# Kernel optimization log

Measured on AMD Instinct MI355X. Metric: run time of the kernel, lower is better.

The kernel has to match this reference:

```python
import jax, jax.numpy as jnp
import numpy as np

B, S, H = 2, 2048, 1024
NH, DH = 16, 64
E, K, F = 8, 2, 4096
EPS = 1e-5


def _ln(x, g, b):
    mu = jnp.mean(x, axis=-1, keepdims=True)
    var = jnp.mean(jnp.square(x - mu), axis=-1, keepdims=True)
    return (x - mu) * jax.lax.rsqrt(var + EPS) * g + b


def setup_inputs() -> dict:
    key = jax.random.key(0)
    ks = jax.random.split(key, 12)
    s = 0.02
    return {
        "x": jax.random.normal(ks[0], (B, S, H), jnp.float32),
        "ln1_g": jnp.ones((H,), jnp.float32),
        "ln1_b": jnp.zeros((H,), jnp.float32),
        "qkv_w": jax.random.normal(ks[1], (3 * H, H), jnp.float32) * s,
        "qkv_b": jnp.zeros((3 * H,), jnp.float32),
        "out_w": jax.random.normal(ks[2], (H, H), jnp.float32) * s,
        "out_b": jnp.zeros((H,), jnp.float32),
        "ln2_g": jnp.ones((H,), jnp.float32),
        "ln2_b": jnp.zeros((H,), jnp.float32),
        "Wg": jax.random.normal(ks[3], (H, E), jnp.float32) * s,
        "W1": jax.random.normal(ks[4], (E, H, F), jnp.float32) * s,
        "b1": jnp.zeros((E, F), jnp.float32),
        "W2": jax.random.normal(ks[5], (E, F, H), jnp.float32) * s,
        "b2": jnp.zeros((E, H), jnp.float32),
    }


def reference(x, ln1_g, ln1_b, qkv_w, qkv_b, out_w, out_b, ln2_g, ln2_b, Wg, W1, b1, W2, b2):
    # ---- LN1 + self-attention + residual (torch MultiheadAttention, no mask) ----
    res = x
    h = _ln(x, ln1_g, ln1_b)
    qkv = h @ qkv_w.T + qkv_b                      # [B,S,3H]
    q, k, v = jnp.split(qkv, 3, axis=-1)
    q = q.reshape(B, S, NH, DH)
    k = k.reshape(B, S, NH, DH)
    v = v.reshape(B, S, NH, DH)
    scores = jnp.einsum("bqhd,bkhd->bhqk", q, k) / jnp.sqrt(jnp.float32(DH))
    attn = jax.nn.softmax(scores, axis=-1)
    o = jnp.einsum("bhqk,bkhd->bqhd", attn, v).reshape(B, S, H)
    x = o @ out_w.T + out_b + res

    # ---- LN2 + MoE FFN + residual ----
    res = x
    h = _ln(x, ln2_g, ln2_b)
    xt = h.reshape(B * S, H)                       # [T,H]
    logits = xt @ Wg                               # [T,E]
    topv, topi = jax.lax.top_k(logits, K)          # [T,K]
    w = jax.nn.softmax(topv, axis=-1)              # renormalized top-k gates
    T = B * S
    gates = jnp.zeros((T, E), xt.dtype).at[jnp.arange(T)[:, None], topi].add(w)
    # dense dispatch: per-expert first GEMM, gate-weighted combine on second
    h1 = jax.nn.gelu(jnp.einsum("th,ehf->tef", xt, W1) + b1)   # [T,E,F]
    y = jnp.einsum("tef,te,efh->th", h1, gates, W2) + gates @ b2
    return y.reshape(B, S, H) + res
```

## Files before the change

kernel.cpp:

```cpp
#include <hip/hip_runtime.h>
#include <hip/hip_bf16.h>

typedef unsigned short u16;
typedef __bf16 bf16x8 __attribute__((ext_vector_type(8)));
typedef float f32x4 __attribute__((ext_vector_type(4)));
typedef __attribute__((address_space(3))) unsigned lds_u32;
typedef __attribute__((address_space(1))) const unsigned gbl_u32;

#define DI __device__ __forceinline__

DI u16 f2b(float f) {
  unsigned u = __builtin_bit_cast(unsigned, f);
  unsigned r = (u + 0x7FFFu + ((u >> 16) & 1u)) >> 16;
  return (u16)r;
}
DI float b2f(u16 h) {
  unsigned u = ((unsigned)h) << 16;
  return __builtin_bit_cast(float, u);
}
DI float wave_sum(float v) {
#pragma unroll
  for (int o = 32; o > 0; o >>= 1) v += __shfl_down(v, o);
  return v;
}
DI float gelu_tanh(float v) {
  float u = 0.7978845608028654f * (v + 0.044715f * v * v * v);
  float eu = __expf(-2.0f * fabsf(u));
  float th = (1.0f - eu) / (1.0f + eu);
  th = (u < 0.0f) ? -th : th;
  return 0.5f * v * (1.0f + th);
}

DI void gld_lds16(const u16* g, u16* l) {
  __builtin_amdgcn_global_load_lds((gbl_u32*)g, (lds_u32*)l, 16, 0, 0);
}

template <int MT, int NT>
DI void gemm_core(const u16* __restrict__ A, long lda, const u16* __restrict__ B,
                  long ldb, int K, u16* As, u16* Bs, f32x4 acc[MT][NT]) {
  const int t = threadIdx.x, lane = t & 63, wave = t >> 6;
  const int wm = (wave >> 1) * (MT * 16), wn = (wave & 1) * (NT * 16);
  const int sr = lane >> 2;
  const int sc = (((lane & 3) ^ ((lane >> 3) & 3)) << 3);
  const int fr = lane & 15;
  const int fk = ((((lane >> 4) ^ ((fr >> 1) & 3))) << 3);
  for (int kb = 0; kb < K; kb += 32) {
#pragma unroll
    for (int ii = 0; ii < MT / 2; ++ii) {
      const int i = ii * 4 + wave;
      gld_lds16(A + (size_t)(i * 16 + sr) * lda + kb + sc, As + i * 512);
    }
#pragma unroll
    for (int ii = 0; ii < NT / 2; ++ii) {
      const int i = ii * 4 + wave;
      gld_lds16(B + (size_t)(i * 16 + sr) * ldb + kb + sc, Bs + i * 512);
    }
    __syncthreads();
    bf16x8 af[MT], bfr[NT];
#pragma unroll
    for (int m = 0; m < MT; ++m)
      af[m] = *(const bf16x8*)(As + (wm + m * 16 + fr) * 32 + fk);
#pragma unroll
    for (int n = 0; n < NT; ++n)
      bfr[n] = *(const bf16x8*)(Bs + (wn + n * 16 + fr) * 32 + fk);
#pragma unroll
    for (int m = 0; m < MT; ++m)
#pragma unroll
      for (int n = 0; n < NT; ++n)
        acc[m][n] =
            __builtin_amdgcn_mfma_f32_16x16x32_bf16(af[m], bfr[n], acc[m][n], 0, 0, 0);
    __syncthreads();
  }
}

constexpr int EP_BF16 = 0;
constexpr int EP_F32RES = 1;

template <int EP, int MT, int NT>
__global__ __launch_bounds__(256) void gemm_k(
    const u16* __restrict__ A, long lda, const u16* __restrict__ B, long ldb,
    const float* __restrict__ bias, float alpha, float* __restrict__ Cf,
    u16* __restrict__ Cb, long ldc, const float* __restrict__ resid, int K) {
  constexpr int BM = MT * 32, BN = NT * 32;
  __shared__ __align__(16) u16 As[BM * 32];
  __shared__ __align__(16) u16 Bs[BN * 32];
  const long m_base = (long)blockIdx.y * BM, n_base = (long)blockIdx.x * BN;
  const u16* Ap = A + m_base * lda;
  const u16* Bp = B + n_base * ldb;
  f32x4 acc[MT][NT];
  const f32x4 z4 = {0.f, 0.f, 0.f, 0.f};
#pragma unroll
  for (int m = 0; m < MT; ++m)
#pragma unroll
    for (int n = 0; n < NT; ++n) acc[m][n] = z4;
  gemm_core<MT, NT>(Ap, lda, Bp, ldb, K, As, Bs, acc);
  const int lane = threadIdx.x & 63, wave = threadIdx.x >> 6;
  const int wm = (wave >> 1) * (MT * 16), wn = (wave & 1) * (NT * 16);
  const int r0 = wm + ((lane >> 4) << 2), c0 = lane & 15;
#pragma unroll
  for (int n = 0; n < NT; ++n) {
    const long gn = n_base + wn + n * 16 + c0;
    const float bv = bias ? bias[gn] : 0.0f;
#pragma unroll
    for (int m = 0; m < MT; ++m)
#pragma unroll
      for (int r = 0; r < 4; ++r) {
        const long gm = m_base + r0 + m * 16 + r;
        const float v = acc[m][n][r] * alpha + bv;
        if (EP == EP_F32RES)
          Cf[gm * ldc + gn] = v + resid[gm * ldc + gn];
        else
          Cb[gm * ldc + gn] = f2b(v);
      }
  }
}

__global__ __launch_bounds__(256) void flash_attn_k(const u16* __restrict__ qkv,
                                                    const u16* __restrict__ Vt,
                                                    u16* __restrict__ O) {
  __shared__ __align__(16) u16 Qs[128 * 64];
  __shared__ __align__(16) u16 Ks[64 * 64];
  __shared__ __align__(16) u16 Vs[64 * 64];
  __shared__ __align__(16) u16 Ps[128 * 72];
  __shared__ __align__(16) float alpha_s[128];
  __shared__ __align__(16) float linv_s[128];
  const int t = threadIdx.x, lane = t & 63, wave = t >> 6;
  const int bh = blockIdx.y, b = bh >> 4, h = bh & 15;
  const int q0 = blockIdx.x << 7;
  const u16* Qg = qkv + ((size_t)(b * 2048 + q0)) * 3072 + h * 64;
  const u16* Kg = qkv + ((size_t)b * 2048) * 3072 + 1024 + h * 64;
  const u16* Vg = Vt + (size_t)bh * 64 * 2048;
  const int sr8 = lane >> 3, sc8 = (((lane & 7) ^ sr8) << 3);
  const int fr = lane & 15, quad = lane >> 4, c0 = fr;
  const int wmS = (wave >> 1) * 32, wnS = (wave & 1) * 64;
  const int wmO = (wave >> 1) * 64, wnO = (wave & 1) * 32;
  const int sq = t >> 1, sh = t & 1;
#pragma unroll
  for (int ii = 0; ii < 4; ++ii) {
    const int i = ii * 4 + wave;
    gld_lds16(Qg + (size_t)(i * 8 + sr8) * 3072 + sc8, Qs + i * 512);
  }
  f32x4 o[4][2];
  const f32x4 z4 = {0.f, 0.f, 0.f, 0.f};
#pragma unroll
  for (int m = 0; m < 4; ++m) {
    o[m][0] = z4;
    o[m][1] = z4;
  }
  float m_run = -1e30f, l_run = 0.0f;
  for (int kv0 = 0; kv0 < 2048; kv0 += 64) {
#pragma unroll
    for (int ii = 0; ii < 2; ++ii) {
      const int i = ii * 4 + wave;
      gld_lds16(Kg + (size_t)(kv0 + i * 8 + sr8) * 3072 + sc8, Ks + i * 512);
      gld_lds16(Vg + (size_t)(i * 8 + sr8) * 2048 + kv0 + sc8, Vs + i * 512);
    }
    __syncthreads();
    f32x4 s[2][4];
#pragma unroll
    for (int m = 0; m < 2; ++m)
#pragma unroll
      for (int n = 0; n < 4; ++n) s[m][n] = z4;
#pragma unroll
    for (int kk = 0; kk < 2; ++kk) {
      bf16x8 ka[2], qb[4];
#pragma unroll
      for (int m = 0; m < 2; ++m) {
        const int row = wmS + m * 16 + fr;
        ka[m] = *(const bf16x8*)(Ks + row * 64 + ((((kk << 2) + quad) ^ (row & 7)) << 3));
      }
#pragma unroll
      for (int n = 0; n < 4; ++n) {
        const int row = wnS + n * 16 + fr;
        qb[n] = *(const bf16x8*)(Qs + row * 64 + ((((kk << 2) + quad) ^ (row & 7)) << 3));
      }
#pragma unroll
      for (int m = 0; m < 2; ++m)
#pragma unroll
        for (int n = 0; n < 4; ++n)
          s[m][n] = __builtin_amdgcn_mfma_f32_16x16x32_bf16(ka[m], qb[n], s[m][n], 0, 0, 0);
    }
#pragma unroll
    for (int m = 0; m < 2; ++m)
#pragma unroll
      for (int n = 0; n < 4; ++n) {
        const int q = wnS + n * 16 + c0;
        const int kv = wmS + m * 16 + (quad << 2);
        ushort4 pk;
        pk.x = f2b(s[m][n][0] * 0.125f);
        pk.y = f2b(s[m][n][1] * 0.125f);
        pk.z = f2b(s[m][n][2] * 0.125f);
        pk.w = f2b(s[m][n][3] * 0.125f);
        *(ushort4*)(Ps + q * 72 + kv) = pk;
      }
    __syncthreads();
    {
      u16* prow = Ps + sq * 72 + (sh << 5);
      uint4 pr[4];
#pragma unroll
      for (int i = 0; i < 4; ++i) pr[i] = *(const uint4*)(prow + i * 8);
      float mloc = -1e30f;
#pragma unroll
      for (int i = 0; i < 4; ++i) {
        const u16* us = (const u16*)&pr[i];
#pragma unroll
        for (int j = 0; j < 8; ++j) mloc = fmaxf(mloc, b2f(us[j]));
      }
      mloc = fmaxf(mloc, __shfl_xor(mloc, 1));
      const float mnew = fmaxf(m_run, mloc);
      const float aa = __expf(m_run - mnew);
      float sloc = 0.0f;
#pragma unroll
      for (int i = 0; i < 4; ++i) {
        u16* us = (u16*)&pr[i];
#pragma unroll
        for (int j = 0; j < 8; ++j) {
          const float pv = __expf(b2f(us[j]) - mnew);
          sloc += pv;
          us[j] = f2b(pv);
        }
      }
#pragma unroll
      for (int i = 0; i < 4; ++i) *(uint4*)(prow + i * 8) = pr[i];
      sloc += __shfl_xor(sloc, 1);
      l_run = l_run * aa + sloc;
      m_run = mnew;
      if (sh == 0) alpha_s[sq] = aa;
    }
    __syncthreads();
#pragma unroll
    for (int m = 0; m < 4; ++m) {
      const f32x4 av = *(const f32x4*)(&alpha_s[wmO + m * 16 + (quad << 2)]);
      o[m][0] *= av;
      o[m][1] *= av;
    }
#pragma unroll
    for (int kk = 0; kk < 2; ++kk) {
      bf16x8 pa[4], vb[2];
#pragma unroll
      for (int m = 0; m < 4; ++m)
        pa[m] = *(const bf16x8*)(Ps + (wmO + m * 16 + fr) * 72 + (kk << 5) + (quad << 3));
#pragma unroll
      for (int n = 0; n < 2; ++n) {
        const int row = wnO + n * 16 + fr;
        vb[n] = *(const bf16x8*)(Vs + row * 64 + ((((kk << 2) + quad) ^ (row & 7)) << 3));
      }
#pragma unroll
      for (int m = 0; m < 4; ++m)
#pragma unroll
        for (int n = 0; n < 2; ++n)
          o[m][n] = __builtin_amdgcn_mfma_f32_16x16x32_bf16(pa[m], vb[n], o[m][n], 0, 0, 0);
    }
    __syncthreads();
  }
  if (sh == 0) linv_s[sq] = 1.0f / l_run;
  __syncthreads();
  u16* Og = O + ((size_t)(b * 2048 + q0)) * 1024 + h * 64;
#pragma unroll
  for (int m = 0; m < 4; ++m) {
    const f32x4 lv = *(const f32x4*)(&linv_s[wmO + m * 16 + (quad << 2)]);
#pragma unroll
    for (int n = 0; n < 2; ++n) {
      const int d = wnO + n * 16 + c0;
#pragma unroll
      for (int r = 0; r < 4; ++r) {
        const int q = wmO + m * 16 + (quad << 2) + r;
        Og[(size_t)q * 1024 + d] = f2b(o[m][n][r] * lv[r]);
      }
    }
  }
}

__global__ __launch_bounds__(256) void moe_gemm1_k(
    const u16* __restrict__ Xg, const u16* __restrict__ W1t,
    const float* __restrict__ b1, const int* __restrict__ counts,
    const int* __restrict__ offs, const int* __restrict__ blk_e,
    const int* __restrict__ blk_m, const int* __restrict__ nblk,
    u16* __restrict__ H1) {
  __shared__ __align__(16) u16 As[128 * 32];
  __shared__ __align__(16) u16 Bs[128 * 32];
  const int by = blockIdx.y;
  if (by >= *nblk) return;
  const int e = blk_e[by], m_base = blk_m[by];
  const int off_e = offs[e];
  const long n_base = (long)blockIdx.x << 7;
  const u16* A = Xg + (size_t)(off_e + m_base) * 1024;
  const u16* B = W1t + (size_t)e * 4096 * 1024 + n_base * 1024;
  f32x4 acc[4][4];
  const f32x4 z4 = {0.f, 0.f, 0.f, 0.f};
#pragma unroll
  for (int m = 0; m < 4; ++m)
#pragma unroll
    for (int n = 0; n < 4; ++n) acc[m][n] = z4;
  gemm_core<4, 4>(A, 1024, B, 1024, 1024, As, Bs, acc);
  const int M_rem = counts[e] - m_base;
  const int lane = threadIdx.x & 63, wave = threadIdx.x >> 6;
  const int wm = (wave >> 1) << 6, wn = (wave & 1) << 6;
  const int r0 = wm + ((lane >> 4) << 2), c0 = lane & 15;
  const float* b1e = b1 + (size_t)e * 4096;
#pragma unroll
  for (int n = 0; n < 4; ++n) {
    const long gn = n_base + wn + n * 16 + c0;
    const float bv = b1e[gn];
#pragma unroll
    for (int m = 0; m < 4; ++m)
#pragma unroll
      for (int r = 0; r < 4; ++r) {
        const int ml = r0 + m * 16 + r;
        if (ml >= M_rem) continue;
        H1[(size_t)(off_e + m_base + ml) * 4096 + gn] = f2b(gelu_tanh(acc[m][n][r] + bv));
      }
  }
}

__global__ __launch_bounds__(256) void moe_gemm2_k(
    const u16* __restrict__ H1, const u16* __restrict__ W2t,
    const int* __restrict__ counts, const int* __restrict__ offs,
    const int* __restrict__ blk_e, const int* __restrict__ blk_m,
    const int* __restrict__ nblk, float* __restrict__ Ye) {
  __shared__ __align__(16) u16 As[128 * 32];
  __shared__ __align__(16) u16 Bs[128 * 32];
  const int by = blockIdx.y;
  if (by >= *nblk) return;
  const int e = blk_e[by], m_base = blk_m[by];
  const int off_e = offs[e];
  const long n_base = (long)blockIdx.x << 7;
  const u16* A = H1 + (size_t)(off_e + m_base) * 4096;
  const u16* B = W2t + (size_t)e * 1024 * 4096 + n_base * 4096;
  f32x4 acc[4][4];
  const f32x4 z4 = {0.f, 0.f, 0.f, 0.f};
#pragma unroll
  for (int m = 0; m < 4; ++m)
#pragma unroll
    for (int n = 0; n < 4; ++n) acc[m][n] = z4;
  gemm_core<4, 4>(A, 4096, B, 4096, 4096, As, Bs, acc);
  const int M_rem = counts[e] - m_base;
  const int lane = threadIdx.x & 63, wave = threadIdx.x >> 6;
  const int wm = (wave >> 1) << 6, wn = (wave & 1) << 6;
  const int r0 = wm + ((lane >> 4) << 2), c0 = lane & 15;
#pragma unroll
  for (int m = 0; m < 4; ++m)
#pragma unroll
    for (int r = 0; r < 4; ++r) {
      const int ml = r0 + m * 16 + r;
      if (ml >= M_rem) continue;
      float* yrow = Ye + (size_t)(off_e + m_base + ml) * 1024 + n_base;
#pragma unroll
      for (int n = 0; n < 4; ++n) yrow[wn + n * 16 + c0] = acc[m][n][r];
    }
}

__global__ __launch_bounds__(256) void ln_k(const float* __restrict__ X,
                                            const float* __restrict__ g,
                                            const float* __restrict__ b,
                                            u16* __restrict__ Y,
                                            float2* __restrict__ stats) {
  const int row = blockIdx.x;
  const float4 xv = ((const float4*)(X + (size_t)row * 1024))[threadIdx.x];
  float s = xv.x + xv.y + xv.z + xv.w;
  float s2 = xv.x * xv.x + xv.y * xv.y + xv.z * xv.z + xv.w * xv.w;
  s = wave_sum(s);
  s2 = wave_sum(s2);
  __shared__ float rs_[4], r2_[4];
  const int lane = threadIdx.x & 63, wave = threadIdx.x >> 6;
  if (lane == 0) { rs_[wave] = s; r2_[wave] = s2; }
  __syncthreads();
  const float tot = rs_[0] + rs_[1] + rs_[2] + rs_[3];
  const float tot2 = r2_[0] + r2_[1] + r2_[2] + r2_[3];
  const float mu = tot * (1.0f / 1024.0f);
  const float var = tot2 * (1.0f / 1024.0f) - mu * mu;
  const float rstd = rsqrtf(var + 1e-5f);
  const float4 gv = ((const float4*)g)[threadIdx.x];
  const float4 bv = ((const float4*)b)[threadIdx.x];
  ushort4 o;
  o.x = f2b((xv.x - mu) * rstd * gv.x + bv.x);
  o.y = f2b((xv.y - mu) * rstd * gv.y + bv.y);
  o.z = f2b((xv.z - mu) * rstd * gv.z + bv.z);
  o.w = f2b((xv.w - mu) * rstd * gv.w + bv.w);
  ((ushort4*)(Y + (size_t)row * 1024))[threadIdx.x] = o;
  if (stats != nullptr && threadIdx.x == 0) stats[row] = make_float2(mu, rstd);
}

__global__ __launch_bounds__(256) void logits_k(
    const float* __restrict__ X2, const float2* __restrict__ stats,
    const float* __restrict__ g, const float* __restrict__ b,
    const float* __restrict__ Wg, float* __restrict__ logits) {
  const int row = blockIdx.x;
  const float2 st = stats[row];
  const float4 xv = ((const float4*)(X2 + (size_t)row * 1024))[threadIdx.x];
  const float4 gv = ((const float4*)g)[threadIdx.x];
  const float4 bv = ((const float4*)b)[threadIdx.x];
  float xt[4];
  xt[0] = (xv.x - st.x) * st.y * gv.x + bv.x;
  xt[1] = (xv.y - st.x) * st.y * gv.y + bv.y;
  xt[2] = (xv.z - st.x) * st.y * gv.z + bv.z;
  xt[3] = (xv.w - st.x) * st.y * gv.w + bv.w;
  float acc[8] = {0, 0, 0, 0, 0, 0, 0, 0};
  const float* w = Wg + (size_t)(threadIdx.x << 2) * 8;
#pragma unroll
  for (int j = 0; j < 4; ++j)
#pragma unroll
    for (int e = 0; e < 8; ++e) acc[e] += xt[j] * w[j * 8 + e];
#pragma unroll
  for (int e = 0; e < 8; ++e) acc[e] = wave_sum(acc[e]);
  __shared__ float red[4][8];
  const int lane = threadIdx.x & 63, wave = threadIdx.x >> 6;
  if (lane == 0) {
#pragma unroll
    for (int e = 0; e < 8; ++e) red[wave][e] = acc[e];
  }
  __syncthreads();
  if (threadIdx.x < 8)
    logits[(size_t)row * 8 + threadIdx.x] = red[0][threadIdx.x] +
        red[1][threadIdx.x] + red[2][threadIdx.x] + red[3][threadIdx.x];
}

__global__ void top2_k(const float* __restrict__ logits, int* __restrict__ topi,
                       float* __restrict__ gatew, int* __restrict__ counts) {
  const int t = blockIdx.x * 256 + threadIdx.x;
  if (t >= 4096) return;
  float l[8];
#pragma unroll
  for (int e = 0; e < 8; ++e) l[e] = logits[(size_t)t * 8 + e];
  int i0 = 0;
  float v0 = l[0];
#pragma unroll
  for (int e = 1; e < 8; ++e)
    if (l[e] > v0) { v0 = l[e]; i0 = e; }
  int i1 = -1;
  float v1 = -1e30f;
#pragma unroll
  for (int e = 0; e < 8; ++e)
    if (e != i0 && l[e] > v1) { v1 = l[e]; i1 = e; }
  const float g0 = 1.0f / (1.0f + __expf(v1 - v0));
  topi[2 * t] = i0;
  topi[2 * t + 1] = i1;
  gatew[2 * t] = g0;
  gatew[2 * t + 1] = 1.0f - g0;
  atomicAdd(&counts[i0], 1);
  atomicAdd(&counts[i1], 1);
}

__global__ void offsets_k(const int* __restrict__ counts, int* __restrict__ offs,
                          int* __restrict__ cursors, int* __restrict__ blk_e,
                          int* __restrict__ blk_m, int* __restrict__ nblk) {
  if (threadIdx.x == 0) {
    int s = 0, nb = 0;
    for (int e = 0; e < 8; ++e) {
      offs[e] = s;
      for (int mb = 0; mb < counts[e]; mb += 128) {
        blk_e[nb] = e;
        blk_m[nb] = mb;
        ++nb;
      }
      s += counts[e];
    }
    *nblk = nb;
  }
  if (threadIdx.x < 8) cursors[threadIdx.x] = 0;
}

__global__ void route_k(const int* __restrict__ topi,
                        const int* __restrict__ offs, int* __restrict__ cursors,
                        int* __restrict__ token_ids, int* __restrict__ tok2slot) {
  const int i = blockIdx.x * 256 + threadIdx.x;
  if (i >= 8192) return;
  const int t = i >> 1;
  const int e = topi[i];
  const int pos = offs[e] + atomicAdd(&cursors[e], 1);
  token_ids[pos] = t;
  tok2slot[i] = pos;
}

__global__ void gather_k(const u16* __restrict__ X,
                         const int* __restrict__ token_ids,
                         u16* __restrict__ Xg) {
  const int i = blockIdx.x * 256 + threadIdx.x;
  const int slot = i >> 7, c = i & 127;
  ((uint4*)Xg)[(size_t)slot * 128 + c] =
      ((const uint4*)X)[(size_t)token_ids[slot] * 128 + c];
}

__global__ void combine_k(const float* __restrict__ X2,
                          const int* __restrict__ topi,
                          const float* __restrict__ gatew,
                          const int* __restrict__ tok2slot,
                          const float* __restrict__ Ye,
                          const float* __restrict__ b2,
                          float* __restrict__ Out) {
  const int t = blockIdx.x;
  float4 v = ((const float4*)(X2 + (size_t)t * 1024))[threadIdx.x];
  const int e0 = topi[2 * t], e1 = topi[2 * t + 1];
  const float g0 = gatew[2 * t], g1 = gatew[2 * t + 1];
  const int s0 = tok2slot[2 * t], s1 = tok2slot[2 * t + 1];
  const float4 y0 = ((const float4*)(Ye + (size_t)s0 * 1024))[threadIdx.x];
  const float4 y1 = ((const float4*)(Ye + (size_t)s1 * 1024))[threadIdx.x];
  const float4 c0 = ((const float4*)(b2 + (size_t)e0 * 1024))[threadIdx.x];
  const float4 c1 = ((const float4*)(b2 + (size_t)e1 * 1024))[threadIdx.x];
  v.x += g0 * (y0.x + c0.x) + g1 * (y1.x + c1.x);
  v.y += g0 * (y0.y + c0.y) + g1 * (y1.y + c1.y);
  v.z += g0 * (y0.z + c0.z) + g1 * (y1.z + c1.z);
  v.w += g0 * (y0.w + c0.w) + g1 * (y1.w + c1.w);
  ((float4*)(Out + (size_t)t * 1024))[threadIdx.x] = v;
}

__global__ void cvt_k(const float* __restrict__ in, u16* __restrict__ out, int n4) {
  const int i = blockIdx.x * 256 + threadIdx.x;
  if (i >= n4) return;
  const float4 v = ((const float4*)in)[i];
  ushort4 o;
  o.x = f2b(v.x);
  o.y = f2b(v.y);
  o.z = f2b(v.z);
  o.w = f2b(v.w);
  ((ushort4*)out)[i] = o;
}

__global__ __launch_bounds__(256) void transpose_cvt_k(
    const float* __restrict__ in, u16* __restrict__ out, int R, int C) {
  __shared__ float tile[32][33];
  const size_t eo = (size_t)blockIdx.z * (size_t)R * C;
  in += eo;
  out += eo;
  const int cb = blockIdx.x << 5, rb = blockIdx.y << 5;
  const int tx = threadIdx.x & 31, ty = threadIdx.x >> 5;
#pragma unroll
  for (int i = 0; i < 4; ++i)
    tile[ty + i * 8][tx] = in[(size_t)(rb + ty + i * 8) * C + cb + tx];
  __syncthreads();
#pragma unroll
  for (int i = 0; i < 4; ++i)
    out[(size_t)(cb + ty + i * 8) * R + rb + tx] = f2b(tile[tx][ty + i * 8]);
}

__global__ __launch_bounds__(256) void vtrans_k(const u16* __restrict__ qkv,
                                                u16* __restrict__ Vt) {
  __shared__ u16 tile[32][33];
  const int z = blockIdx.z, b = z >> 4, h = z & 15;
  const int sb = blockIdx.x << 5;
  const int db = blockIdx.y << 5;
  const int tx = threadIdx.x & 31, ty = threadIdx.x >> 5;
  const u16* src = qkv + ((size_t)b * 2048) * 3072 + 2048 + h * 64;
#pragma unroll
  for (int i = 0; i < 4; ++i)
    tile[ty + i * 8][tx] = src[(size_t)(sb + ty + i * 8) * 3072 + db + tx];
  __syncthreads();
  u16* dst = Vt + ((size_t)z * 64 + db) * 2048 + sb;
#pragma unroll
  for (int i = 0; i < 4; ++i)
    dst[(size_t)(ty + i * 8) * 2048 + tx] = tile[tx][ty + i * 8];
}

__global__ void zero_k(int* __restrict__ counts) {
  if (threadIdx.x < 8) counts[threadIdx.x] = 0;
}

extern "C" void kernel_launch(void* const* d_in, const int* in_sizes, int n_in,
                              void* d_out, int out_size, void* d_ws,
                              size_t ws_size, hipStream_t stream) {
  (void)in_sizes; (void)n_in; (void)out_size;
  const float* x = (const float*)d_in[0];
  const float* ln1_g = (const float*)d_in[1];
  const float* ln1_b = (const float*)d_in[2];
  const float* qkv_w = (const float*)d_in[3];
  const float* qkv_b = (const float*)d_in[4];
  const float* out_w = (const float*)d_in[5];
  const float* out_b = (const float*)d_in[6];
  const float* ln2_g = (const float*)d_in[7];
  const float* ln2_b = (const float*)d_in[8];
  const float* Wg = (const float*)d_in[9];
  const float* W1 = (const float*)d_in[10];
  const float* b1 = (const float*)d_in[11];
  const float* W2 = (const float*)d_in[12];
  const float* b2 = (const float*)d_in[13];
  float* out = (float*)d_out;

  const int T = 4096, H = 1024, F = 4096, E = 8;

  char* p = (char*)d_ws;
  auto alloc = [&](size_t n) {
    char* r = p;
    p += (n + 255) & ~(size_t)255;
    return r;
  };
  u16* qkvw_bf = (u16*)alloc((size_t)3 * H * H * 2);
  u16* outw_bf = (u16*)alloc((size_t)H * H * 2);
  u16* W1t = (u16*)alloc((size_t)E * F * H * 2);
  u16* W2t = (u16*)alloc((size_t)E * H * F * 2);
  u16* h1bf = (u16*)alloc((size_t)T * H * 2);
  u16* qkvbf = (u16*)alloc((size_t)T * 3 * H * 2);
  u16* obf = (u16*)alloc((size_t)T * H * 2);
  float* x2 = (float*)alloc((size_t)T * H * 4);
  u16* H1 = (u16*)alloc((size_t)(2 * T + 128) * F * 2);
  float* Ye = (float*)alloc((size_t)2 * T * H * 4);
  u16* Xg = (u16*)alloc((size_t)(2 * T + 128) * H * 2);
  float* logits = (float*)alloc((size_t)T * E * 4);
  float2* stats = (float2*)alloc((size_t)T * 8);
  int* topi = (int*)alloc((size_t)T * 2 * 4);
  float* gatew = (float*)alloc((size_t)T * 2 * 4);
  int* counts = (int*)alloc(64);
  int* offs = (int*)alloc(64);
  int* cursors = (int*)alloc(64);
  int* blk_e = (int*)alloc(512);
  int* blk_m = (int*)alloc(512);
  int* nblk = (int*)alloc(64);
  int* token_ids = (int*)alloc((size_t)(2 * T + 128) * 4);
  int* tok2slot = (int*)alloc((size_t)2 * T * 4);
  if ((size_t)(p - (char*)d_ws) > ws_size) return;

  u16* Vt = h1bf;
  u16* h2bf = obf;

  zero_k<<<1, 64, 0, stream>>>(counts);
  cvt_k<<<3 * H * H / 4 / 256, 256, 0, stream>>>(qkv_w, qkvw_bf, 3 * H * H / 4);
  cvt_k<<<H * H / 4 / 256, 256, 0, stream>>>(out_w, outw_bf, H * H / 4);
  transpose_cvt_k<<<dim3(F / 32, H / 32, E), 256, 0, stream>>>(W1, W1t, H, F);
  transpose_cvt_k<<<dim3(H / 32, F / 32, E), 256, 0, stream>>>(W2, W2t, F, H);

  ln_k<<<T, 256, 0, stream>>>(x, ln1_g, ln1_b, h1bf, nullptr);

  gemm_k<EP_BF16, 4, 4><<<dim3(3 * H / 128, T / 128), 256, 0, stream>>>(
      h1bf, H, qkvw_bf, H, qkv_b, 1.0f, nullptr, qkvbf, 3 * H, nullptr, H);

  vtrans_k<<<dim3(2048 / 32, 2, 32), 256, 0, stream>>>(qkvbf, Vt);

  flash_attn_k<<<dim3(2048 / 128, 32), 256, 0, stream>>>(qkvbf, Vt, obf);

  gemm_k<EP_F32RES, 4, 4><<<dim3(H / 128, T / 128), 256, 0, stream>>>(
      obf, H, outw_bf, H, out_b, 1.0f, x2, nullptr, H, x, H);

  ln_k<<<T, 256, 0, stream>>>(x2, ln2_g, ln2_b, h2bf, stats);
  logits_k<<<T, 256, 0, stream>>>(x2, stats, ln2_g, ln2_b, Wg, logits);
  top2_k<<<T / 256, 256, 0, stream>>>(logits, topi, gatew, counts);
  offsets_k<<<1, 64, 0, stream>>>(counts, offs, cursors, blk_e, blk_m, nblk);
  route_k<<<2 * T / 256, 256, 0, stream>>>(topi, offs, cursors, token_ids,
                                           tok2slot);
  gather_k<<<2 * T * (H / 8) / 256, 256, 0, stream>>>(h2bf, token_ids, Xg);

  moe_gemm1_k<<<dim3(F / 128, 72), 256, 0, stream>>>(Xg, W1t, b1, counts, offs,
                                                     blk_e, blk_m, nblk, H1);
  moe_gemm2_k<<<dim3(H / 128, 72), 256, 0, stream>>>(H1, W2t, counts, offs,
                                                     blk_e, blk_m, nblk, Ye);

  combine_k<<<T, 256, 0, stream>>>(x2, topi, gatew, tok2slot, Ye, b2, out);
}
```

Baseline: 992.4 us.

## Split-K the out-projection and MoE down GEMMs and halve attention query tile

The output-projection GEMM is split into two K halves that write fp32 partials, and a new reduce kernel adds bias and residual. The second MoE GEMM is likewise split into two K halves, writing to two partial buffers; the combine kernel sums them. Flash attention now uses 64-query tiles instead of 128, doubling the block count. The goal is to fill more compute units on small grids, at the cost of extra fp32 partial-buffer traffic, one extra launch, and less K/V reuse per attention block. Partial buffers reuse dead workspace regions (h1bf/qkvbf and H1).

```diff
diff --git a/kernel.cpp b/kernel.cpp
--- a/kernel.cpp
+++ b/kernel.cpp
@@ -73,77 +73,117 @@
   }
 }
 
-constexpr int EP_BF16 = 0;
-constexpr int EP_F32RES = 1;
-
-template <int EP, int MT, int NT>
+template <int MT, int NT>
 __global__ __launch_bounds__(256) void gemm_k(
     const u16* __restrict__ A, long lda, const u16* __restrict__ B, long ldb,
-    const float* __restrict__ bias, float alpha, float* __restrict__ Cf,
-    u16* __restrict__ Cb, long ldc, const float* __restrict__ resid, int K) {
+    const float* __restrict__ bias, u16* __restrict__ Cb, long ldc, int K) {
   constexpr int BM = MT * 32, BN = NT * 32;
   __shared__ __align__(16) u16 As[BM * 32];
   __shared__ __align__(16) u16 Bs[BN * 32];
   const long m_base = (long)blockIdx.y * BM, n_base = (long)blockIdx.x * BN;
-  const u16* Ap = A + m_base * lda;
-  const u16* Bp = B + n_base * ldb;
   f32x4 acc[MT][NT];
   const f32x4 z4 = {0.f, 0.f, 0.f, 0.f};
 #pragma unroll
   for (int m = 0; m < MT; ++m)
 #pragma unroll
     for (int n = 0; n < NT; ++n) acc[m][n] = z4;
-  gemm_core<MT, NT>(Ap, lda, Bp, ldb, K, As, Bs, acc);
+  gemm_core<MT, NT>(A + m_base * lda, lda, B + n_base * ldb, ldb, K, As, Bs, acc);
   const int lane = threadIdx.x & 63, wave = threadIdx.x >> 6;
   const int wm = (wave >> 1) * (MT * 16), wn = (wave & 1) * (NT * 16);
   const int r0 = wm + ((lane >> 4) << 2), c0 = lane & 15;
 #pragma unroll
   for (int n = 0; n < NT; ++n) {
     const long gn = n_base + wn + n * 16 + c0;
-    const float bv = bias ? bias[gn] : 0.0f;
+    const float bv = bias[gn];
 #pragma unroll
     for (int m = 0; m < MT; ++m)
 #pragma unroll
       for (int r = 0; r < 4; ++r) {
         const long gm = m_base + r0 + m * 16 + r;
-        const float v = acc[m][n][r] * alpha + bv;
-        if (EP == EP_F32RES)
-          Cf[gm * ldc + gn] = v + resid[gm * ldc + gn];
-        else
-          Cb[gm * ldc + gn] = f2b(v);
-      }
-  }
+        Cb[gm * ldc + gn] = f2b(acc[m][n][r] + bv);
+      }
+  }
+}
+
+template <int MT, int NT>
+__global__ __launch_bounds__(256) void gemm_pk_k(
+    const u16* __restrict__ A, long lda, const u16* __restrict__ B, long ldb,
+    float* __restrict__ Cp, long M, long N, int K_per) {
+  constexpr int BM = MT * 32, BN = NT * 32;
+  __shared__ __align__(16) u16 As[BM * 32];
+  __shared__ __align__(16) u16 Bs[BN * 32];
+  const long m_base = (long)blockIdx.y * BM, n_base = (long)blockIdx.x * BN;
+  const long k0 = (long)blockIdx.z * K_per;
+  f32x4 acc[MT][NT];
+  const f32x4 z4 = {0.f, 0.f, 0.f, 0.f};
+#pragma unroll
+  for (int m = 0; m < MT; ++m)
+#pragma unroll
+    for (int n = 0; n < NT; ++n) acc[m][n] = z4;
+  gemm_core<MT, NT>(A + m_base * lda + k0, lda, B + n_base * ldb + k0, ldb,
+                    K_per, As, Bs, acc);
+  float* C = Cp + (size_t)blockIdx.z * M * N;
+  const int lane = threadIdx.x & 63, wave = threadIdx.x >> 6;
+  const int wm = (wave >> 1) * (MT * 16), wn = (wave & 1) * (NT * 16);
+  const int r0 = wm + ((lane >> 4) << 2), c0 = lane & 15;
+#pragma unroll
+  for (int m = 0; m < MT; ++m)
+#pragma unroll
+    for (int r = 0; r < 4; ++r) {
+      const long gm = m_base + r0 + m * 16 + r;
+      float* crow = C + gm * N + n_base;
+#pragma unroll
+      for (int n = 0; n < NT; ++n) crow[wn + n * 16 + c0] = acc[m][n][r];
+    }
+}
+
+__global__ void reduce2_k(const float* __restrict__ P0,
+                          const float* __restrict__ P1,
+                          const float* __restrict__ bias,
+                          const float* __restrict__ resid,
+                          float* __restrict__ X2) {
+  const size_t row = blockIdx.x;
+  const int c = threadIdx.x;
+  const float4 a = ((const float4*)(P0 + row * 1024))[c];
+  const float4 b = ((const float4*)(P1 + row * 1024))[c];
+  const float4 bb = ((const float4*)bias)[c];
+  const float4 rr = ((const float4*)(resid + row * 1024))[c];
+  float4 v;
+  v.x = a.x + b.x + bb.x + rr.x;
+  v.y = a.y + b.y + bb.y + rr.y;
+  v.z = a.z + b.z + bb.z + rr.z;
+  v.w = a.w + b.w + bb.w + rr.w;
+  ((float4*)(X2 + row * 1024))[c] = v;
 }
 
 __global__ __launch_bounds__(256) void flash_attn_k(const u16* __restrict__ qkv,
                                                     const u16* __restrict__ Vt,
                                                     u16* __restrict__ O) {
-  __shared__ __align__(16) u16 Qs[128 * 64];
+  __shared__ __align__(16) u16 Qs[64 * 64];
   __shared__ __align__(16) u16 Ks[64 * 64];
   __shared__ __align__(16) u16 Vs[64 * 64];
-  __shared__ __align__(16) u16 Ps[128 * 72];
-  __shared__ __align__(16) float alpha_s[128];
-  __shared__ __align__(16) float linv_s[128];
+  __shared__ __align__(16) u16 Ps[64 * 72];
+  __shared__ __align__(16) float alpha_s[64];
+  __shared__ __align__(16) float linv_s[64];
   const int t = threadIdx.x, lane = t & 63, wave = t >> 6;
+  const int wr = wave >> 1, wc = wave & 1;
   const int bh = blockIdx.y, b = bh >> 4, h = bh & 15;
-  const int q0 = blockIdx.x << 7;
+  const int q0 = blockIdx.x << 6;
   const u16* Qg = qkv + ((size_t)(b * 2048 + q0)) * 3072 + h * 64;
   const u16* Kg = qkv + ((size_t)b * 2048) * 3072 + 1024 + h * 64;
   const u16* Vg = Vt + (size_t)bh * 64 * 2048;
   const int sr8 = lane >> 3, sc8 = (((lane & 7) ^ sr8) << 3);
   const int fr = lane & 15, quad = lane >> 4, c0 = fr;
-  const int wmS = (wave >> 1) * 32, wnS = (wave & 1) * 64;
-  const int wmO = (wave >> 1) * 64, wnO = (wave & 1) * 32;
-  const int sq = t >> 1, sh = t & 1;
-#pragma unroll
-  for (int ii = 0; ii < 4; ++ii) {
+  const int sq = t >> 2, sh = t & 3;
+#pragma unroll
+  for (int ii = 0; ii < 2; ++ii) {
     const int i = ii * 4 + wave;
     gld_lds16(Qg + (size_t)(i * 8 + sr8) * 3072 + sc8, Qs + i * 512);
   }
-  f32x4 o[4][2];
+  f32x4 o[2][2];
   const f32x4 z4 = {0.f, 0.f, 0.f, 0.f};
 #pragma unroll
-  for (int m = 0; m < 4; ++m) {
+  for (int m = 0; m < 2; ++m) {
     o[m][0] = z4;
     o[m][1] = z4;
   }
@@ -156,36 +196,36 @@
       gld_lds16(Vg + (size_t)(i * 8 + sr8) * 2048 + kv0 + sc8, Vs + i * 512);
     }
     __syncthreads();
-    f32x4 s[2][4];
+    f32x4 s[2][2];
 #pragma unroll
     for (int m = 0; m < 2; ++m)
 #pragma unroll
-      for (int n = 0; n < 4; ++n) s[m][n] = z4;
+      for (int n = 0; n < 2; ++n) s[m][n] = z4;
 #pragma unroll
     for (int kk = 0; kk < 2; ++kk) {
-      bf16x8 ka[2], qb[4];
+      bf16x8 ka[2], qb[2];
 #pragma unroll
       for (int m = 0; m < 2; ++m) {
-        const int row = wmS + m * 16 + fr;
+        const int row = wr * 32 + m * 16 + fr;
         ka[m] = *(const bf16x8*)(Ks + row * 64 + ((((kk << 2) + quad) ^ (row & 7)) << 3));
       }
 #pragma unroll
-      for (int n = 0; n < 4; ++n) {
-        const int row = wnS + n * 16 + fr;
+      for (int n = 0; n < 2; ++n) {
+        const int row = wc * 32 + n * 16 + fr;
         qb[n] = *(const bf16x8*)(Qs + row * 64 + ((((kk << 2) + quad) ^ (row & 7)) << 3));
       }
 #pragma unroll
       for (int m = 0; m < 2; ++m)
 #pragma unroll
-        for (int n = 0; n < 4; ++n)
+        for (int n = 0; n < 2; ++n)
           s[m][n] = __builtin_amdgcn_mfma_f32_16x16x32_bf16(ka[m], qb[n], s[m][n], 0, 0, 0);
     }
 #pragma unroll
     for (int m = 0; m < 2; ++m)
 #pragma unroll
-      for (int n = 0; n < 4; ++n) {
-        const int q = wnS + n * 16 + c0;
-        const int kv = wmS + m * 16 + (quad << 2);
+      for (int n = 0; n < 2; ++n) {
+        const int q = wc * 32 + n * 16 + c0;
+        const int kv = wr * 32 + m * 16 + (quad << 2);
         ushort4 pk;
         pk.x = f2b(s[m][n][0] * 0.125f);
         pk.y = f2b(s[m][n][1] * 0.125f);
@@ -195,23 +235,24 @@
       }
     __syncthreads();
     {
-      u16* prow = Ps + sq * 72 + (sh << 5);
-      uint4 pr[4];
-#pragma unroll
-      for (int i = 0; i < 4; ++i) pr[i] = *(const uint4*)(prow + i * 8);
+      u16* prow = Ps + sq * 72 + (sh << 4);
+      uint4 pr[2];
+#pragma unroll
+      for (int i = 0; i < 2; ++i) pr[i] = *(const uint4*)(prow + i * 8);
       float mloc = -1e30f;
 #pragma unroll
-      for (int i = 0; i < 4; ++i) {
+      for (int i = 0; i < 2; ++i) {
         const u16* us = (const u16*)&pr[i];
 #pragma unroll
         for (int j = 0; j < 8; ++j) mloc = fmaxf(mloc, b2f(us[j]));
       }
       mloc = fmaxf(mloc, __shfl_xor(mloc, 1));
+      mloc = fmaxf(mloc, __shfl_xor(mloc, 2));
       const float mnew = fmaxf(m_run, mloc);
       const float aa = __expf(m_run - mnew);
       float sloc = 0.0f;
 #pragma unroll
-      for (int i = 0; i < 4; ++i) {
+      for (int i = 0; i < 2; ++i) {
         u16* us = (u16*)&pr[i];
 #pragma unroll
         for (int j = 0; j < 8; ++j) {
@@ -221,32 +262,33 @@
         }
       }
 #pragma unroll
-      for (int i = 0; i < 4; ++i) *(uint4*)(prow + i * 8) = pr[i];
+      for (int i = 0; i < 2; ++i) *(uint4*)(prow + i * 8) = pr[i];
       sloc += __shfl_xor(sloc, 1);
+      sloc += __shfl_xor(sloc, 2);
       l_run = l_run * aa + sloc;
       m_run = mnew;
       if (sh == 0) alpha_s[sq] = aa;
     }
     __syncthreads();
 #pragma unroll
-    for (int m = 0; m < 4; ++m) {
-      const f32x4 av = *(const f32x4*)(&alpha_s[wmO + m * 16 + (quad << 2)]);
+    for (int m = 0; m < 2; ++m) {
+      const f32x4 av = *(const f32x4*)(&alpha_s[wr * 32 + m * 16 + (quad << 2)]);
       o[m][0] *= av;
       o[m][1] *= av;
     }
 #pragma unroll
     for (int kk = 0; kk < 2; ++kk) {
-      bf16x8 pa[4], vb[2];
-#pragma unroll
-      for (int m = 0; m < 4; ++m)
-        pa[m] = *(const bf16x8*)(Ps + (wmO + m * 16 + fr) * 72 + (kk << 5) + (quad << 3));
+      bf16x8 pa[2], vb[2];
+#pragma unroll
+      for (int m = 0; m < 2; ++m)
+        pa[m] = *(const bf16x8*)(Ps + (wr * 32 + m * 16 + fr) * 72 + (kk << 5) + (quad << 3));
 #pragma unroll
       for (int n = 0; n < 2; ++n) {
-        const int row = wnO + n * 16 + fr;
+        const int row = wc * 32 + n * 16 + fr;
         vb[n] = *(const bf16x8*)(Vs + row * 64 + ((((kk << 2) + quad) ^ (row & 7)) << 3));
       }
 #pragma unroll
-      for (int m = 0; m < 4; ++m)
+      for (int m = 0; m < 2; ++m)
 #pragma unroll
         for (int n = 0; n < 2; ++n)
           o[m][n] = __builtin_amdgcn_mfma_f32_16x16x32_bf16(pa[m], vb[n], o[m][n], 0, 0, 0);
@@ -257,14 +299,14 @@
   __syncthreads();
   u16* Og = O + ((size_t)(b * 2048 + q0)) * 1024 + h * 64;
 #pragma unroll
-  for (int m = 0; m < 4; ++m) {
-    const f32x4 lv = *(const f32x4*)(&linv_s[wmO + m * 16 + (quad << 2)]);
+  for (int m = 0; m < 2; ++m) {
+    const f32x4 lv = *(const f32x4*)(&linv_s[wr * 32 + m * 16 + (quad << 2)]);
 #pragma unroll
     for (int n = 0; n < 2; ++n) {
-      const int d = wnO + n * 16 + c0;
+      const int d = wc * 32 + n * 16 + c0;
 #pragma unroll
       for (int r = 0; r < 4; ++r) {
-        const int q = wmO + m * 16 + (quad << 2) + r;
+        const int q = wr * 32 + m * 16 + (quad << 2) + r;
         Og[(size_t)q * 1024 + d] = f2b(o[m][n][r] * lv[r]);
       }
     }
@@ -317,7 +359,8 @@
     const u16* __restrict__ H1, const u16* __restrict__ W2t,
     const int* __restrict__ counts, const int* __restrict__ offs,
     const int* __restrict__ blk_e, const int* __restrict__ blk_m,
-    const int* __restrict__ nblk, float* __restrict__ Ye) {
+    const int* __restrict__ nblk, float* __restrict__ Yp0,
+    float* __restrict__ Yp1) {
   __shared__ __align__(16) u16 As[128 * 32];
   __shared__ __align__(16) u16 Bs[128 * 32];
   const int by = blockIdx.y;
@@ -325,15 +368,18 @@
   const int e = blk_e[by], m_base = blk_m[by];
   const int off_e = offs[e];
   const long n_base = (long)blockIdx.x << 7;
-  const u16* A = H1 + (size_t)(off_e + m_base) * 4096;
-  const u16* B = W2t + (size_t)e * 1024 * 4096 + n_base * 4096;
+  const int kz = blockIdx.z;
+  const long k0 = (long)kz * 2048;
+  const u16* A = H1 + (size_t)(off_e + m_base) * 4096 + k0;
+  const u16* B = W2t + (size_t)e * 1024 * 4096 + n_base * 4096 + k0;
   f32x4 acc[4][4];
   const f32x4 z4 = {0.f, 0.f, 0.f, 0.f};
 #pragma unroll
   for (int m = 0; m < 4; ++m)
 #pragma unroll
     for (int n = 0; n < 4; ++n) acc[m][n] = z4;
-  gemm_core<4, 4>(A, 4096, B, 4096, 4096, As, Bs, acc);
+  gemm_core<4, 4>(A, 4096, B, 4096, 2048, As, Bs, acc);
+  float* Yp = kz ? Yp1 : Yp0;
   const int M_rem = counts[e] - m_base;
   const int lane = threadIdx.x & 63, wave = threadIdx.x >> 6;
   const int wm = (wave >> 1) << 6, wn = (wave & 1) << 6;
@@ -344,7 +390,7 @@
     for (int r = 0; r < 4; ++r) {
       const int ml = r0 + m * 16 + r;
       if (ml >= M_rem) continue;
-      float* yrow = Ye + (size_t)(off_e + m_base + ml) * 1024 + n_base;
+      float* yrow = Yp + (size_t)(off_e + m_base + ml) * 1024 + n_base;
 #pragma unroll
       for (int n = 0; n < 4; ++n) yrow[wn + n * 16 + c0] = acc[m][n][r];
     }
@@ -485,23 +531,27 @@
                           const int* __restrict__ topi,
                           const float* __restrict__ gatew,
                           const int* __restrict__ tok2slot,
-                          const float* __restrict__ Ye,
+                          const float* __restrict__ Yp0,
+                          const float* __restrict__ Yp1,
                           const float* __restrict__ b2,
                           float* __restrict__ Out) {
   const int t = blockIdx.x;
-  float4 v = ((const float4*)(X2 + (size_t)t * 1024))[threadIdx.x];
+  const int c = threadIdx.x;
+  float4 v = ((const float4*)(X2 + (size_t)t * 1024))[c];
   const int e0 = topi[2 * t], e1 = topi[2 * t + 1];
   const float g0 = gatew[2 * t], g1 = gatew[2 * t + 1];
   const int s0 = tok2slot[2 * t], s1 = tok2slot[2 * t + 1];
-  const float4 y0 = ((const float4*)(Ye + (size_t)s0 * 1024))[threadIdx.x];
-  const float4 y1 = ((const float4*)(Ye + (size_t)s1 * 1024))[threadIdx.x];
-  const float4 c0 = ((const float4*)(b2 + (size_t)e0 * 1024))[threadIdx.x];
-  const float4 c1 = ((const float4*)(b2 + (size_t)e1 * 1024))[threadIdx.x];
-  v.x += g0 * (y0.x + c0.x) + g1 * (y1.x + c1.x);
-  v.y += g0 * (y0.y + c0.y) + g1 * (y1.y + c1.y);
-  v.z += g0 * (y0.z + c0.z) + g1 * (y1.z + c1.z);
-  v.w += g0 * (y0.w + c0.w) + g1 * (y1.w + c1.w);
-  ((float4*)(Out + (size_t)t * 1024))[threadIdx.x] = v;
+  const float4 ya0 = ((const float4*)(Yp0 + (size_t)s0 * 1024))[c];
+  const float4 yb0 = ((const float4*)(Yp1 + (size_t)s0 * 1024))[c];
+  const float4 ya1 = ((const float4*)(Yp0 + (size_t)s1 * 1024))[c];
+  const float4 yb1 = ((const float4*)(Yp1 + (size_t)s1 * 1024))[c];
+  const float4 c0 = ((const float4*)(b2 + (size_t)e0 * 1024))[c];
+  const float4 c1 = ((const float4*)(b2 + (size_t)e1 * 1024))[c];
+  v.x += g0 * (ya0.x + yb0.x + c0.x) + g1 * (ya1.x + yb1.x + c1.x);
+  v.y += g0 * (ya0.y + yb0.y + c0.y) + g1 * (ya1.y + yb1.y + c1.y);
+  v.z += g0 * (ya0.z + yb0.z + c0.z) + g1 * (ya1.z + yb1.z + c1.z);
+  v.w += g0 * (ya0.w + yb0.w + c0.w) + g1 * (ya1.w + yb1.w + c1.w);
+  ((float4*)(Out + (size_t)t * 1024))[c] = v;
 }
 
 __global__ void cvt_k(const float* __restrict__ in, u16* __restrict__ out, int n4) {
@@ -592,7 +642,7 @@
   u16* obf = (u16*)alloc((size_t)T * H * 2);
   float* x2 = (float*)alloc((size_t)T * H * 4);
   u16* H1 = (u16*)alloc((size_t)(2 * T + 128) * F * 2);
-  float* Ye = (float*)alloc((size_t)2 * T * H * 4);
+  float* Yp0 = (float*)alloc((size_t)2 * T * H * 4);
   u16* Xg = (u16*)alloc((size_t)(2 * T + 128) * H * 2);
   float* logits = (float*)alloc((size_t)T * E * 4);
   float2* stats = (float2*)alloc((size_t)T * 8);
@@ -610,6 +660,8 @@
 
   u16* Vt = h1bf;
   u16* h2bf = obf;
+  float* Yp1 = (float*)h1bf;
+  float* Po = (float*)H1;
 
   zero_k<<<1, 64, 0, stream>>>(counts);
   cvt_k<<<3 * H * H / 4 / 256, 256, 0, stream>>>(qkv_w, qkvw_bf, 3 * H * H / 4);
@@ -619,15 +671,16 @@
 
   ln_k<<<T, 256, 0, stream>>>(x, ln1_g, ln1_b, h1bf, nullptr);
 
-  gemm_k<EP_BF16, 4, 4><<<dim3(3 * H / 128, T / 128), 256, 0, stream>>>(
-      h1bf, H, qkvw_bf, H, qkv_b, 1.0f, nullptr, qkvbf, 3 * H, nullptr, H);
+  gemm_k<4, 4><<<dim3(3 * H / 128, T / 128), 256, 0, stream>>>(
+      h1bf, H, qkvw_bf, H, qkv_b, qkvbf, 3 * H, H);
 
   vtrans_k<<<dim3(2048 / 32, 2, 32), 256, 0, stream>>>(qkvbf, Vt);
 
-  flash_attn_k<<<dim3(2048 / 128, 32), 256, 0, stream>>>(qkvbf, Vt, obf);
-
-  gemm_k<EP_F32RES, 4, 4><<<dim3(H / 128, T / 128), 256, 0, stream>>>(
-      obf, H, outw_bf, H, out_b, 1.0f, x2, nullptr, H, x, H);
+  flash_attn_k<<<dim3(2048 / 64, 32), 256, 0, stream>>>(qkvbf, Vt, obf);
+
+  gemm_pk_k<4, 4><<<dim3(H / 128, T / 128, 2), 256, 0, stream>>>(
+      obf, H, outw_bf, H, Po, T, H, 512);
+  reduce2_k<<<T, 256, 0, stream>>>(Po, Po + (size_t)T * H, out_b, x, x2);
 
   ln_k<<<T, 256, 0, stream>>>(x2, ln2_g, ln2_b, h2bf, stats);
   logits_k<<<T, 256, 0, stream>>>(x2, stats, ln2_g, ln2_b, Wg, logits);
@@ -639,8 +692,9 @@
 
   moe_gemm1_k<<<dim3(F / 128, 72), 256, 0, stream>>>(Xg, W1t, b1, counts, offs,
                                                      blk_e, blk_m, nblk, H1);
-  moe_gemm2_k<<<dim3(H / 128, 72), 256, 0, stream>>>(H1, W2t, counts, offs,
-                                                     blk_e, blk_m, nblk, Ye);
-
-  combine_k<<<T, 256, 0, stream>>>(x2, topi, gatew, tok2slot, Ye, b2, out);
-}
+  moe_gemm2_k<<<dim3(H / 128, 72, 2), 256, 0, stream>>>(H1, W2t, counts, offs,
+                                                        blk_e, blk_m, nblk,
+                                                        Yp0, Yp1);
+
+  combine_k<<<T, 256, 0, stream>>>(x2, topi, gatew, tok2slot, Yp0, Yp1, b2, out);
+}
```

After: 966.0 us. -2.7%, faster.
